# Performance work log

Hardware: AMD Instinct MI355X
Metric: run time of the kernel (lower is better)

## Reference

```python
import jax, jax.numpy as jnp
import numpy as np

EPS = 1e-7  # K.epsilon()

def squash(s, axis=-1):
    # v = (||s||^2 / (1 + ||s||^2)) * s / ||s||
    sq = jnp.sum(jnp.square(s), axis=axis, keepdims=True)
    scale = sq / (1.0 + sq) / jnp.sqrt(sq + EPS)
    return scale * s

def setup_inputs() -> dict:
    key = jax.random.key(0)
    k1, k2, k3 = jax.random.split(key, 3)
    B, J, P = 128, 2048, 8      # batch, input_num_capsule, input_dim_capsule
    N, D = 32, 16               # num_capsule, dim_capsule
    x = jax.random.normal(k1, (B, J, P), dtype=jnp.float32)
    W = jax.random.normal(k2, (N, J, D, P), dtype=jnp.float32) * 0.1
    bias = jax.random.normal(k3, (N, D), dtype=jnp.float32) * 0.1
    return {"x": x, "W": W, "bias": bias}

def reference(x, W, bias):
    # x: [B, J, P], W: [N, J, D, P], bias: [N, D]
    routings = 3
    # inputs_hat[b,n,j,d] = sum_p W[n,j,d,p] * x[b,j,p]   -> [B, N, J, D]
    u_hat = jnp.einsum('njdp,bjp->bnjd', W, x)
    B_, N, J, _ = u_hat.shape
    b = jnp.zeros((B_, N, J), dtype=u_hat.dtype)
    outputs = None
    for i in range(routings):
        c = jax.nn.softmax(b, axis=1)                      # coupling over output caps
        s = jnp.einsum('bnj,bnjd->bnd', c, u_hat) + bias   # weighted sum + bias
        outputs = squash(s)                                # [B, N, D]
        if i < routings - 1:
            b = b + jnp.einsum('bnd,bnjd->bnj', outputs, u_hat)  # agreement
    return outputs
```

## Files before the change

### kernel.cpp

```cpp
#include <hip/hip_runtime.h>
#include <hip/hip_bf16.h>

#define B_   128
#define J_   2048
#define N_   32
#define D_   16
#define NJC  32

typedef __attribute__((ext_vector_type(8))) short short8b;
typedef __attribute__((ext_vector_type(4))) float f32x4;
typedef __attribute__((ext_vector_type(16))) float f32x16;

__device__ inline short bf16s(float f) {
    union { __hip_bfloat16 h; short s; } u;
    u.h = __float2bfloat16(f);
    return u.s;
}


__global__ __launch_bounds__(256) void capsW(const float* __restrict__ W,
                                             __hip_bfloat16* __restrict__ Wbf,
                                             __hip_bfloat16* __restrict__ Wt) {
    __shared__ float lds[16 * 132];
    const int t = threadIdx.x;
    const size_t base = (size_t)blockIdx.x * 2048;
    const int r  = t >> 4;
    const int e0 = (t & 15) * 8;

    float4 a = *(const float4*)(W + base + t * 8);
    float4 b = *(const float4*)(W + base + t * 8 + 4);
    short8b w8;
    w8[0]=bf16s(a.x); w8[1]=bf16s(a.y); w8[2]=bf16s(a.z); w8[3]=bf16s(a.w);
    w8[4]=bf16s(b.x); w8[5]=bf16s(b.y); w8[6]=bf16s(b.z); w8[7]=bf16s(b.w);
    *(short8b*)((short*)Wbf + base + t * 8) = w8;
    *(float4*)&lds[r * 132 + e0]     = a;
    *(float4*)&lds[r * 132 + e0 + 4] = b;
    __syncthreads();

    short8b o8;
    #pragma unroll
    for (int k = 0; k < 8; ++k) {
        int q = e0 + k;
        int p = q >> 4, d = q & 15;
        o8[k] = bf16s(lds[r * 132 + d * 8 + p]);
    }
    *(short8b*)((short*)Wt + base + t * 8) = o8;
}

__global__ __launch_bounds__(256) void capsT(const float* __restrict__ x,
                                             float* __restrict__ xT) {
    __shared__ float tile[32 * 260 + 4];
    const int t  = threadIdx.x;
    const int jt = blockIdx.x & 63;
    const int bt = blockIdx.x >> 6;
    const int j0 = jt * 32, b0 = bt * 32;

    for (int idx = t; idx < 2048; idx += 256) {
        int bl = idx >> 6, f4 = idx & 63;
        float4 v = *(const float4*)(x + (size_t)(b0 + bl) * 16384 + j0 * 8 + f4 * 4);
        *(float4*)&tile[bl * 260 + f4 * 4] = v;
    }
    __syncthreads();
    for (int idx = t; idx < 2048; idx += 256) {
        int jj = idx >> 6, f4o = idx & 63;
        int bl = f4o >> 1, po = (f4o & 1) * 4;
        float4 v = *(const float4*)&tile[bl * 260 + jj * 8 + po];
        *(float4*)(xT + ((size_t)(j0 + jj) * 128 + b0 + bl) * 8 + po) = v;
    }
}

__global__ __launch_bounds__(256) void capsA(const __hip_bfloat16* __restrict__ Wbf,
                                             const float* __restrict__ xT,
                                             const __hip_bfloat16* __restrict__ cT,
                                             float* __restrict__ s_part,
                                             int mode) {
    const int t     = threadIdx.x;
    const int lane  = t & 63;
    const int i     = blockIdx.x;
    const int jc    = (i & 7) + 8 * (i >> 8);
    const int n     = (i >> 3) & 31;
    const int wv    = t >> 6;
    const int colid = lane & 15;
    const int kgrp  = lane >> 4;

    const int b0 = wv * 32 + colid;
    const int b1 = b0 + 16;

    f32x4 acc0 = {0.f, 0.f, 0.f, 0.f};
    f32x4 acc1 = {0.f, 0.f, 0.f, 0.f};

    for (int ks = 0; ks < 16; ++ks) {
        const int j = jc * 64 + ks * 4 + kgrp;

        short8b bfrag = *(const short8b*)((const short*)Wbf
                          + (((size_t)n * J_ + j) * 16 + colid) * 8);

        float c0 = 1.0f / 32.0f, c1 = 1.0f / 32.0f;
        if (mode) {
            c0 = __bfloat162float(cT[((size_t)n * J_ + j) * B_ + b0]);
            c1 = __bfloat162float(cT[((size_t)n * J_ + j) * B_ + b1]);
        }

        const float4* xp0 = (const float4*)(xT + ((size_t)j * 128 + b0) * 8);
        float4 xa = xp0[0], xb = xp0[1];
        short8b afrag0;
        afrag0[0] = bf16s(xa.x * c0); afrag0[1] = bf16s(xa.y * c0);
        afrag0[2] = bf16s(xa.z * c0); afrag0[3] = bf16s(xa.w * c0);
        afrag0[4] = bf16s(xb.x * c0); afrag0[5] = bf16s(xb.y * c0);
        afrag0[6] = bf16s(xb.z * c0); afrag0[7] = bf16s(xb.w * c0);

        const float4* xp1 = (const float4*)(xT + ((size_t)j * 128 + b1) * 8);
        float4 xe = xp1[0], xf = xp1[1];
        short8b afrag1;
        afrag1[0] = bf16s(xe.x * c1); afrag1[1] = bf16s(xe.y * c1);
        afrag1[2] = bf16s(xe.z * c1); afrag1[3] = bf16s(xe.w * c1);
        afrag1[4] = bf16s(xf.x * c1); afrag1[5] = bf16s(xf.y * c1);
        afrag1[6] = bf16s(xf.z * c1); afrag1[7] = bf16s(xf.w * c1);

        acc0 = __builtin_amdgcn_mfma_f32_16x16x32_bf16(afrag0, bfrag, acc0, 0, 0, 0);
        acc1 = __builtin_amdgcn_mfma_f32_16x16x32_bf16(afrag1, bfrag, acc1, 0, 0, 0);
    }

    float* sdst = s_part + (size_t)jc * (B_ * N_ * D_);
    #pragma unroll
    for (int r = 0; r < 4; ++r) {
        int brow = wv * 32 + kgrp * 4 + r;
        sdst[(size_t)brow * 512 + n * 16 + colid]        = acc0[r];
        sdst[(size_t)(brow + 16) * 512 + n * 16 + colid] = acc1[r];
    }
}

__global__ __launch_bounds__(256) void capsR(const float* __restrict__ s_part,
                                             const float* __restrict__ bias,
                                             float* __restrict__ out,
                                             __hip_bfloat16* __restrict__ oT) {
    int gid = blockIdx.x * 256 + threadIdx.x;
    float sv = bias[gid & 511];
    #pragma unroll
    for (int jc = 0; jc < NJC; ++jc)
        sv += s_part[(size_t)jc * 65536 + gid];
    float sq = sv * sv;
    sq += __shfl_xor(sq, 1);
    sq += __shfl_xor(sq, 2);
    sq += __shfl_xor(sq, 4);
    sq += __shfl_xor(sq, 8);
    float scale = sq / (1.0f + sq) / sqrtf(sq + 1e-7f);
    float ov = scale * sv;
    out[gid] = ov;
    int b = gid >> 9, nd = gid & 511;
    int n = nd >> 4, d = nd & 15;
    oT[((size_t)n * B_ + b) * D_ + d] = __float2bfloat16(ov);
}

__global__ __launch_bounds__(256) void capsB(const __hip_bfloat16* __restrict__ Wt,
                                             const float* __restrict__ xT,
                                             const __hip_bfloat16* __restrict__ oT,
                                             __hip_bfloat16* __restrict__ blogT,
                                             int accumulate) {
    const int t    = threadIdx.x;
    const int lane = t & 63;
    const int i    = blockIdx.x;
    const int xcd  = i & 7;
    const int r    = i >> 3;
    const int jq   = xcd * 64 + (r & 63);
    const int nh   = r >> 6;
    const int j0   = jq * 4;
    const int wv   = t >> 6;
    const int g    = lane >> 5;
    const int col  = lane & 31;
    const int b    = wv * 32 + col;

    const int jlA = (col >> 4) + 2 * ((col >> 2) & 1);
    const int pA  = 4 * ((col >> 3) & 1) + (col & 3);

    float4 xv[4];
    #pragma unroll
    for (int jloc = 0; jloc < 2; ++jloc)
        #pragma unroll
        for (int h = 0; h < 2; ++h)
            xv[jloc * 2 + h] = *(const float4*)(xT
                + ((size_t)(j0 + 2 * g + jloc) * 128 + b) * 8 + h * 4);

    const short* wtBase = (const short*)Wt
        + (((size_t)(nh * 16) * J_ + j0 + jlA) * 8 + pA) * 16 + g * 8;
    const short* oBase  = (const short*)oT
        + ((size_t)(nh * 16) * B_ + b) * 16 + g * 8;
    const __hip_bfloat16* blogBase0 = blogT
        + ((size_t)(nh * 16) * J_ + j0 + 2 * g) * B_ + b;
    const __hip_bfloat16* blogBase1 = blogBase0 + B_;

    f32x16 zz;
    #pragma unroll
    for (int q = 0; q < 16; ++q) zz[q] = 0.0f;

    short8b af[4], bf[4];
    float   od0[4], od1[4];
    #pragma unroll
    for (int k = 0; k < 4; ++k) {
        af[k] = *(const short8b*)(wtBase + (size_t)k * (J_ * 128));
        bf[k] = *(const short8b*)(oBase  + (size_t)k * (B_ * 16));
        if (accumulate) {
            od0[k] = __bfloat162float(blogBase0[(size_t)k * (J_ * B_)]);
            od1[k] = __bfloat162float(blogBase1[(size_t)k * (J_ * B_)]);
        }
    }

    #pragma unroll
    for (int nn = 0; nn < 16; ++nn) {
        const int n = nh * 16 + nn;
        short8b afrag = af[nn & 3];
        short8b bfrag = bf[nn & 3];
        float old0 = od0[nn & 3], old1 = od1[nn & 3];
        if (nn + 4 < 16) {
            af[nn & 3] = *(const short8b*)(wtBase + (size_t)(nn + 4) * (J_ * 128));
            bf[nn & 3] = *(const short8b*)(oBase  + (size_t)(nn + 4) * (B_ * 16));
            if (accumulate) {
                od0[nn & 3] = __bfloat162float(blogBase0[(size_t)(nn + 4) * (J_ * B_)]);
                od1[nn & 3] = __bfloat162float(blogBase1[(size_t)(nn + 4) * (J_ * B_)]);
            }
        }

        f32x16 acc =
            __builtin_amdgcn_mfma_f32_32x32x16_bf16(afrag, bfrag, zz, 0, 0, 0);

        float t0 = acc[0] * xv[0].x + acc[1] * xv[0].y
                 + acc[2] * xv[0].z + acc[3] * xv[0].w
                 + acc[4] * xv[1].x + acc[5] * xv[1].y
                 + acc[6] * xv[1].z + acc[7] * xv[1].w;
        float t1 = acc[8]  * xv[2].x + acc[9]  * xv[2].y
                 + acc[10] * xv[2].z + acc[11] * xv[2].w
                 + acc[12] * xv[3].x + acc[13] * xv[3].y
                 + acc[14] * xv[3].z + acc[15] * xv[3].w;
        if (accumulate) { t0 += old0; t1 += old1; }

        size_t a0 = ((size_t)n * J_ + j0 + 2 * g) * B_ + b;
        blogT[a0]      = __float2bfloat16(t0);
        blogT[a0 + B_] = __float2bfloat16(t1);
    }
}

__global__ __launch_bounds__(256) void capsD(const __hip_bfloat16* __restrict__ blogT,
                                             __hip_bfloat16* __restrict__ cT) {
    int gid = blockIdx.x * 256 + threadIdx.x;
    float v[32];
    float m = -1e30f;
    #pragma unroll
    for (int nn = 0; nn < 32; ++nn) {
        v[nn] = __bfloat162float(blogT[(size_t)nn * (J_ * B_) + gid]);
        m = fmaxf(m, v[nn]);
    }
    float sum = 0.0f;
    #pragma unroll
    for (int nn = 0; nn < 32; ++nn) sum += __expf(v[nn] - m);
    float inv = 1.0f / sum;
    #pragma unroll
    for (int nn = 0; nn < 32; ++nn)
        cT[(size_t)nn * (J_ * B_) + gid] = __float2bfloat16(__expf(v[nn] - m) * inv);
}

extern "C" void kernel_launch(void* const* d_in, const int* in_sizes, int n_in,
                              void* d_out, int out_size, void* d_ws, size_t ws_size,
                              hipStream_t stream) {
    const float* x    = (const float*)d_in[0];
    const float* W    = (const float*)d_in[1];
    const float* bias = (const float*)d_in[2];
    float* out = (float*)d_out;

    float* ws = (float*)d_ws;
    float*           xT     = ws;
    __hip_bfloat16*  blogT  = (__hip_bfloat16*)(ws + 2097152);
    __hip_bfloat16*  cT     = (__hip_bfloat16*)(ws + 6291456);
    float*           s_part = ws + 10485760;
    __hip_bfloat16*  oT     = (__hip_bfloat16*)(ws + 12582912);
    __hip_bfloat16*  Wbf    = (__hip_bfloat16*)(ws + 12615680);
    __hip_bfloat16*  Wt     = (__hip_bfloat16*)(ws + 16809984);

    dim3 b256(256);

    capsW<<<dim3(4096), b256, 0, stream>>>(W, Wbf, Wt);
    capsT<<<dim3(256),  b256, 0, stream>>>(x, xT);

    capsA<<<dim3(1024), b256, 0, stream>>>(Wbf, xT, cT, s_part, 0);
    capsR<<<dim3(256),  b256, 0, stream>>>(s_part, bias, out, oT);
    capsB<<<dim3(1024), b256, 0, stream>>>(Wt, xT, oT, blogT, 0);

    capsD<<<dim3(1024), b256, 0, stream>>>(blogT, cT);
    capsA<<<dim3(1024), b256, 0, stream>>>(Wbf, xT, cT, s_part, 1);
    capsR<<<dim3(256),  b256, 0, stream>>>(s_part, bias, out, oT);
    capsB<<<dim3(1024), b256, 0, stream>>>(Wt, xT, oT, blogT, 1);

    capsD<<<dim3(1024), b256, 0, stream>>>(blogT, cT);
    capsA<<<dim3(1024), b256, 0, stream>>>(Wbf, xT, cT, s_part, 1);
    capsR<<<dim3(256),  b256, 0, stream>>>(s_part, bias, out, oT);
}
```

Measured before the change: 121.2 us.

## Merge W/x prep kernels and retile capsA to four capsules per block

Merges the W conversion and x transpose kernels into one launch that branches on block index, saving one launch. capsA now has each block cover four output capsules over 32 j values, so each x fragment is reused across four MFMA pairs, and the j range is split into 64 chunks with the block index mapped across XCDs. This doubles the number of s_part partials that capsR must reduce, moves the workspace offsets to fit them, and raises register use for the unrolled accumulators.

```diff
diff --git a/kernel.cpp b/kernel.cpp
--- a/kernel.cpp
+++ b/kernel.cpp
@@ -5,7 +5,7 @@
 #define J_   2048
 #define N_   32
 #define D_   16
-#define NJC  32
+#define NJC  64
 
 typedef __attribute__((ext_vector_type(8))) short short8b;
 typedef __attribute__((ext_vector_type(4))) float f32x4;
@@ -18,54 +18,55 @@
 }
 
 
-__global__ __launch_bounds__(256) void capsW(const float* __restrict__ W,
+__global__ __launch_bounds__(256) void capsP(const float* __restrict__ W,
                                              __hip_bfloat16* __restrict__ Wbf,
-                                             __hip_bfloat16* __restrict__ Wt) {
-    __shared__ float lds[16 * 132];
+                                             __hip_bfloat16* __restrict__ Wt,
+                                             const float* __restrict__ x,
+                                             float* __restrict__ xT) {
+    __shared__ float lds[32 * 260 + 4];
     const int t = threadIdx.x;
-    const size_t base = (size_t)blockIdx.x * 2048;
-    const int r  = t >> 4;
-    const int e0 = (t & 15) * 8;
-
-    float4 a = *(const float4*)(W + base + t * 8);
-    float4 b = *(const float4*)(W + base + t * 8 + 4);
-    short8b w8;
-    w8[0]=bf16s(a.x); w8[1]=bf16s(a.y); w8[2]=bf16s(a.z); w8[3]=bf16s(a.w);
-    w8[4]=bf16s(b.x); w8[5]=bf16s(b.y); w8[6]=bf16s(b.z); w8[7]=bf16s(b.w);
-    *(short8b*)((short*)Wbf + base + t * 8) = w8;
-    *(float4*)&lds[r * 132 + e0]     = a;
-    *(float4*)&lds[r * 132 + e0 + 4] = b;
-    __syncthreads();
-
-    short8b o8;
-    #pragma unroll
-    for (int k = 0; k < 8; ++k) {
-        int q = e0 + k;
-        int p = q >> 4, d = q & 15;
-        o8[k] = bf16s(lds[r * 132 + d * 8 + p]);
-    }
-    *(short8b*)((short*)Wt + base + t * 8) = o8;
-}
-
-__global__ __launch_bounds__(256) void capsT(const float* __restrict__ x,
-                                             float* __restrict__ xT) {
-    __shared__ float tile[32 * 260 + 4];
-    const int t  = threadIdx.x;
-    const int jt = blockIdx.x & 63;
-    const int bt = blockIdx.x >> 6;
-    const int j0 = jt * 32, b0 = bt * 32;
-
-    for (int idx = t; idx < 2048; idx += 256) {
-        int bl = idx >> 6, f4 = idx & 63;
-        float4 v = *(const float4*)(x + (size_t)(b0 + bl) * 16384 + j0 * 8 + f4 * 4);
-        *(float4*)&tile[bl * 260 + f4 * 4] = v;
-    }
-    __syncthreads();
-    for (int idx = t; idx < 2048; idx += 256) {
-        int jj = idx >> 6, f4o = idx & 63;
-        int bl = f4o >> 1, po = (f4o & 1) * 4;
-        float4 v = *(const float4*)&tile[bl * 260 + jj * 8 + po];
-        *(float4*)(xT + ((size_t)(j0 + jj) * 128 + b0 + bl) * 8 + po) = v;
+
+    if (blockIdx.x < 4096) {
+        const size_t base = (size_t)blockIdx.x * 2048;
+        const int r  = t >> 4;
+        const int e0 = (t & 15) * 8;
+
+        float4 a = *(const float4*)(W + base + t * 8);
+        float4 b = *(const float4*)(W + base + t * 8 + 4);
+        short8b w8;
+        w8[0]=bf16s(a.x); w8[1]=bf16s(a.y); w8[2]=bf16s(a.z); w8[3]=bf16s(a.w);
+        w8[4]=bf16s(b.x); w8[5]=bf16s(b.y); w8[6]=bf16s(b.z); w8[7]=bf16s(b.w);
+        *(short8b*)((short*)Wbf + base + t * 8) = w8;
+        *(float4*)&lds[r * 132 + e0]     = a;
+        *(float4*)&lds[r * 132 + e0 + 4] = b;
+        __syncthreads();
+
+        short8b o8;
+        #pragma unroll
+        for (int k = 0; k < 8; ++k) {
+            int q = e0 + k;
+            int p = q >> 4, d = q & 15;
+            o8[k] = bf16s(lds[r * 132 + d * 8 + p]);
+        }
+        *(short8b*)((short*)Wt + base + t * 8) = o8;
+    } else {
+        const int bid = blockIdx.x - 4096;
+        const int jt = bid & 63;
+        const int bt = bid >> 6;
+        const int j0 = jt * 32, b0 = bt * 32;
+
+        for (int idx = t; idx < 2048; idx += 256) {
+            int bl = idx >> 6, f4 = idx & 63;
+            float4 v = *(const float4*)(x + (size_t)(b0 + bl) * 16384 + j0 * 8 + f4 * 4);
+            *(float4*)&lds[bl * 260 + f4 * 4] = v;
+        }
+        __syncthreads();
+        for (int idx = t; idx < 2048; idx += 256) {
+            int jj = idx >> 6, f4o = idx & 63;
+            int bl = f4o >> 1, po = (f4o & 1) * 4;
+            float4 v = *(const float4*)&lds[bl * 260 + jj * 8 + po];
+            *(float4*)(xT + ((size_t)(j0 + jj) * 128 + b0 + bl) * 8 + po) = v;
+        }
     }
 }
 
@@ -77,8 +78,11 @@
     const int t     = threadIdx.x;
     const int lane  = t & 63;
     const int i     = blockIdx.x;
-    const int jc    = (i & 7) + 8 * (i >> 8);
-    const int n     = (i >> 3) & 31;
+    const int xcd   = i & 7;
+    const int r     = i >> 3;
+    const int jc    = xcd * 8 + (r & 7);
+    const int ng    = r >> 3;
+    const int n0    = ng * 4;
     const int wv    = t >> 6;
     const int colid = lane & 15;
     const int kgrp  = lane >> 4;
@@ -86,47 +90,61 @@
     const int b0 = wv * 32 + colid;
     const int b1 = b0 + 16;
 
-    f32x4 acc0 = {0.f, 0.f, 0.f, 0.f};
-    f32x4 acc1 = {0.f, 0.f, 0.f, 0.f};
-
-    for (int ks = 0; ks < 16; ++ks) {
-        const int j = jc * 64 + ks * 4 + kgrp;
-
-        short8b bfrag = *(const short8b*)((const short*)Wbf
-                          + (((size_t)n * J_ + j) * 16 + colid) * 8);
-
-        float c0 = 1.0f / 32.0f, c1 = 1.0f / 32.0f;
-        if (mode) {
-            c0 = __bfloat162float(cT[((size_t)n * J_ + j) * B_ + b0]);
-            c1 = __bfloat162float(cT[((size_t)n * J_ + j) * B_ + b1]);
-        }
+    f32x4 acc[4][2];
+    #pragma unroll
+    for (int nn = 0; nn < 4; ++nn) {
+        acc[nn][0] = (f32x4){0.f, 0.f, 0.f, 0.f};
+        acc[nn][1] = (f32x4){0.f, 0.f, 0.f, 0.f};
+    }
+
+    #pragma unroll
+    for (int ks = 0; ks < 8; ++ks) {
+        const int j = jc * 32 + ks * 4 + kgrp;
 
         const float4* xp0 = (const float4*)(xT + ((size_t)j * 128 + b0) * 8);
         float4 xa = xp0[0], xb = xp0[1];
-        short8b afrag0;
-        afrag0[0] = bf16s(xa.x * c0); afrag0[1] = bf16s(xa.y * c0);
-        afrag0[2] = bf16s(xa.z * c0); afrag0[3] = bf16s(xa.w * c0);
-        afrag0[4] = bf16s(xb.x * c0); afrag0[5] = bf16s(xb.y * c0);
-        afrag0[6] = bf16s(xb.z * c0); afrag0[7] = bf16s(xb.w * c0);
-
         const float4* xp1 = (const float4*)(xT + ((size_t)j * 128 + b1) * 8);
         float4 xe = xp1[0], xf = xp1[1];
-        short8b afrag1;
-        afrag1[0] = bf16s(xe.x * c1); afrag1[1] = bf16s(xe.y * c1);
-        afrag1[2] = bf16s(xe.z * c1); afrag1[3] = bf16s(xe.w * c1);
-        afrag1[4] = bf16s(xf.x * c1); afrag1[5] = bf16s(xf.y * c1);
-        afrag1[6] = bf16s(xf.z * c1); afrag1[7] = bf16s(xf.w * c1);
-
-        acc0 = __builtin_amdgcn_mfma_f32_16x16x32_bf16(afrag0, bfrag, acc0, 0, 0, 0);
-        acc1 = __builtin_amdgcn_mfma_f32_16x16x32_bf16(afrag1, bfrag, acc1, 0, 0, 0);
+
+        #pragma unroll
+        for (int nn = 0; nn < 4; ++nn) {
+            const int n = n0 + nn;
+
+            short8b bfrag = *(const short8b*)((const short*)Wbf
+                              + (((size_t)n * J_ + j) * 16 + colid) * 8);
+
+            float c0 = 1.0f / 32.0f, c1 = 1.0f / 32.0f;
+            if (mode) {
+                c0 = __bfloat162float(cT[((size_t)n * J_ + j) * B_ + b0]);
+                c1 = __bfloat162float(cT[((size_t)n * J_ + j) * B_ + b1]);
+            }
+
+            short8b afrag0;
+            afrag0[0] = bf16s(xa.x * c0); afrag0[1] = bf16s(xa.y * c0);
+            afrag0[2] = bf16s(xa.z * c0); afrag0[3] = bf16s(xa.w * c0);
+            afrag0[4] = bf16s(xb.x * c0); afrag0[5] = bf16s(xb.y * c0);
+            afrag0[6] = bf16s(xb.z * c0); afrag0[7] = bf16s(xb.w * c0);
+
+            short8b afrag1;
+            afrag1[0] = bf16s(xe.x * c1); afrag1[1] = bf16s(xe.y * c1);
+            afrag1[2] = bf16s(xe.z * c1); afrag1[3] = bf16s(xe.w * c1);
+            afrag1[4] = bf16s(xf.x * c1); afrag1[5] = bf16s(xf.y * c1);
+            afrag1[6] = bf16s(xf.z * c1); afrag1[7] = bf16s(xf.w * c1);
+
+            acc[nn][0] = __builtin_amdgcn_mfma_f32_16x16x32_bf16(afrag0, bfrag, acc[nn][0], 0, 0, 0);
+            acc[nn][1] = __builtin_amdgcn_mfma_f32_16x16x32_bf16(afrag1, bfrag, acc[nn][1], 0, 0, 0);
+        }
     }
 
     float* sdst = s_part + (size_t)jc * (B_ * N_ * D_);
     #pragma unroll
-    for (int r = 0; r < 4; ++r) {
-        int brow = wv * 32 + kgrp * 4 + r;
-        sdst[(size_t)brow * 512 + n * 16 + colid]        = acc0[r];
-        sdst[(size_t)(brow + 16) * 512 + n * 16 + colid] = acc1[r];
+    for (int nn = 0; nn < 4; ++nn) {
+        #pragma unroll
+        for (int rr = 0; rr < 4; ++rr) {
+            int brow = wv * 32 + kgrp * 4 + rr;
+            sdst[(size_t)brow * 512 + (n0 + nn) * 16 + colid]        = acc[nn][0][rr];
+            sdst[(size_t)(brow + 16) * 512 + (n0 + nn) * 16 + colid] = acc[nn][1][rr];
+        }
     }
 }
 
@@ -271,25 +289,24 @@
     __hip_bfloat16*  blogT  = (__hip_bfloat16*)(ws + 2097152);
     __hip_bfloat16*  cT     = (__hip_bfloat16*)(ws + 6291456);
     float*           s_part = ws + 10485760;
-    __hip_bfloat16*  oT     = (__hip_bfloat16*)(ws + 12582912);
-    __hip_bfloat16*  Wbf    = (__hip_bfloat16*)(ws + 12615680);
-    __hip_bfloat16*  Wt     = (__hip_bfloat16*)(ws + 16809984);
+    __hip_bfloat16*  oT     = (__hip_bfloat16*)(ws + 14680064);
+    __hip_bfloat16*  Wbf    = (__hip_bfloat16*)(ws + 14712832);
+    __hip_bfloat16*  Wt     = (__hip_bfloat16*)(ws + 18907136);
 
     dim3 b256(256);
 
-    capsW<<<dim3(4096), b256, 0, stream>>>(W, Wbf, Wt);
-    capsT<<<dim3(256),  b256, 0, stream>>>(x, xT);
-
-    capsA<<<dim3(1024), b256, 0, stream>>>(Wbf, xT, cT, s_part, 0);
+    capsP<<<dim3(4352), b256, 0, stream>>>(W, Wbf, Wt, x, xT);
+
+    capsA<<<dim3(512),  b256, 0, stream>>>(Wbf, xT, cT, s_part, 0);
     capsR<<<dim3(256),  b256, 0, stream>>>(s_part, bias, out, oT);
     capsB<<<dim3(1024), b256, 0, stream>>>(Wt, xT, oT, blogT, 0);
 
     capsD<<<dim3(1024), b256, 0, stream>>>(blogT, cT);
-    capsA<<<dim3(1024), b256, 0, stream>>>(Wbf, xT, cT, s_part, 1);
+    capsA<<<dim3(512),  b256, 0, stream>>>(Wbf, xT, cT, s_part, 1);
     capsR<<<dim3(256),  b256, 0, stream>>>(s_part, bias, out, oT);
     capsB<<<dim3(1024), b256, 0, stream>>>(Wt, xT, oT, blogT, 1);
 
     capsD<<<dim3(1024), b256, 0, stream>>>(blogT, cT);
-    capsA<<<dim3(1024), b256, 0, stream>>>(Wbf, xT, cT, s_part, 1);
+    capsA<<<dim3(512),  b256, 0, stream>>>(Wbf, xT, cT, s_part, 1);
     capsR<<<dim3(256),  b256, 0, stream>>>(s_part, bias, out, oT);
 }
```

New measurement: 155.2 us. +28.1%, slower.
